# Optimization experiments

Measured on AMD Instinct MI355X. Metric: run time of the kernel, lower is better.

Reference implementation:

```python
import jax, jax.numpy as jnp
import numpy as np

EPS = 1e-8
TAU = 0.2  # gumbel temperature


def lorentz_linear(x, W, log_scale):
    # y = W x; project back onto hyperboloid (k=1): time from sigmoid, rescale space
    y = x @ W.T
    time = jax.nn.sigmoid(y[..., :1]) * jnp.exp(log_scale) + 1.1
    narrow = y[..., 1:]
    s = (time * time - 1.0) / jnp.clip(jnp.sum(narrow * narrow, axis=-1, keepdims=True), EPS, None)
    return jnp.concatenate([time, narrow * jnp.sqrt(s)], axis=-1)


def logmap0(x):
    # Lorentz (k=1) log map at origin o=(1,0,...,0): (0, arccosh(x0) * xs/||xs||)
    x0 = x[..., :1]
    xs = x[..., 1:]
    nrm = jnp.clip(jnp.linalg.norm(xs, axis=-1, keepdims=True), EPS, None)
    d = jnp.arccosh(jnp.clip(x0, 1.0 + 1e-6, None))
    return jnp.concatenate([jnp.zeros_like(x0), d * xs / nrm], axis=-1)


def lorentz_dist(a, b):
    # dist = arccosh(-<a,b>_L), <a,b>_L = -a0*b0 + sum_i ai*bi
    inner = a[..., 0] * b[..., 0] - jnp.sum(a[..., 1:] * b[..., 1:], axis=-1)
    return jnp.arccosh(jnp.clip(inner, 1.0 + 1e-6, None))


def scatter_softmax(score, seg, num_segments):
    m = jax.ops.segment_max(score, seg, num_segments=num_segments)
    m = jnp.where(jnp.isfinite(m), m, 0.0)  # empty segments
    e = jnp.exp(score - m[seg])
    s = jax.ops.segment_sum(e, seg, num_segments=num_segments)
    return e / jnp.clip(s[seg], EPS, None)


def setup_inputs() -> dict:
    key = jax.random.key(0)
    ks = jax.random.split(key, 8)
    N, E, D, A = 50000, 800000, 128, 128
    # nodes on hyperboloid: time = sqrt(1 + ||space||^2)
    xs = jax.random.normal(ks[0], (N, D - 1), dtype=jnp.float32)
    x0 = jnp.sqrt(1.0 + jnp.sum(xs * xs, axis=-1, keepdims=True))
    x = jnp.concatenate([x0, xs], axis=-1)
    src = jax.random.randint(ks[1], (E,), 0, N)
    dst = jax.random.randint(ks[2], (E,), 0, N)
    edge_value = jax.random.uniform(ks[3], (E,), dtype=jnp.float32)
    stdv = 1.0 / np.sqrt(D)
    Wq = jax.random.uniform(ks[4], (D, D), minval=-stdv, maxval=stdv, dtype=jnp.float32).at[:, 0].set(0.0)
    Wk = jax.random.uniform(ks[5], (D, D), minval=-stdv, maxval=stdv, dtype=jnp.float32).at[:, 0].set(0.0)
    Wa = jax.random.normal(ks[6], (A, D), dtype=jnp.float32) * np.sqrt(2.0 / (A + D))
    log_scale = jnp.asarray(np.log(10.0), dtype=jnp.float32)
    return {"x": x, "src": src, "dst": dst, "edge_value": edge_value,
            "Wq": Wq, "Wk": Wk, "Wa": Wa,
            "log_scale_q": log_scale, "log_scale_k": log_scale}


def reference(x, src, dst, edge_value, Wq, Wk, Wa, log_scale_q, log_scale_k):
    N = x.shape[0]
    # assignment logits in tangent space -> softmax
    ass = jax.nn.softmax(logmap0(x) @ Wa.T, axis=-1)  # [N, A]
    q = lorentz_linear(x, Wq, log_scale_q)            # [N, D]
    k = lorentz_linear(x, Wk, log_scale_k)
    # per-edge negative Lorentz distance
    score = -lorentz_dist(q[src], k[dst])             # [E]
    # scatter softmax over outgoing edges of each src node
    score = scatter_softmax(score, src, N)
    # sparse attention matmul: out[i] = sum_{e: src=i} score_e * ass[dst_e]
    ass = jax.ops.segment_sum(score[:, None] * ass[dst], src, num_segments=N)  # [N, A]
    # gumbel softmax on log(ass + 1e-6)
    logits = jnp.log(ass + 1e-6)
    u = jax.random.uniform(jax.random.key(42), logits.shape, minval=1e-10, maxval=1.0)
    g = -jnp.log(-jnp.log(u))
    return jax.nn.softmax((logits + g) / TAU, axis=-1)
```

## Files before the change

### kernel.cpp

```cpp
#include <hip/hip_runtime.h>
#include <hip/hip_bf16.h>
#include <hip/hip_fp16.h>
#include <math.h>


#define D128 128
#define XP 136

typedef _Float16 f16x2 __attribute__((ext_vector_type(2)));
typedef _Float16 f16x8 __attribute__((ext_vector_type(8)));
typedef float f32x4 __attribute__((ext_vector_type(4)));

union U4 { uint4 u; f16x2 f2[4]; __half2 hh[4]; };

__device__ __forceinline__ void threefry2x32(unsigned x0, unsigned x1,
                                             unsigned& o0, unsigned& o1) {
  const unsigned k0 = 0u, k1 = 42u;
  const unsigned k2 = 0x1BD11BDAu ^ k0 ^ k1;
  x0 += k0; x1 += k1;
#define TF_ROT(r) { x0 += x1; x1 = (x1 << (r)) | (x1 >> (32 - (r))); x1 ^= x0; }
  TF_ROT(13) TF_ROT(15) TF_ROT(26) TF_ROT(6)
  x0 += k1; x1 += k2 + 1u;
  TF_ROT(17) TF_ROT(29) TF_ROT(16) TF_ROT(24)
  x0 += k2; x1 += k0 + 2u;
  TF_ROT(13) TF_ROT(15) TF_ROT(26) TF_ROT(6)
  x0 += k0; x1 += k1 + 3u;
  TF_ROT(17) TF_ROT(29) TF_ROT(16) TF_ROT(24)
  x0 += k1; x1 += k2 + 4u;
  TF_ROT(13) TF_ROT(15) TF_ROT(26) TF_ROT(6)
  x0 += k2; x1 += k0 + 5u;
#undef TF_ROT
  o0 = x0; o1 = x1;
}

__global__ __launch_bounds__(256) void cvt_count_kernel(
    const float* __restrict__ Wq, const float* __restrict__ Wk,
    const float* __restrict__ Wa, __half* __restrict__ wqh,
    __half* __restrict__ wkh, __half* __restrict__ wah,
    const int* __restrict__ src, int* __restrict__ counts, int E) {
  int b = blockIdx.x;
  if (b < 24) {
    int i = b * 256 + threadIdx.x;
    int w = i >> 11, r = i & 2047;
    if (w >= 3) return;
    size_t off = (size_t)r * 8;
    const float* s = (w == 0) ? Wq : (w == 1) ? Wk : Wa;
    __half* d = (w == 0) ? wqh : (w == 1) ? wkh : wah;
    float4 a = *reinterpret_cast<const float4*>(s + off);
    float4 c = *reinterpret_cast<const float4*>(s + off + 4);
    union { __half2 h2[4]; uint4 u; } pk;
    pk.h2[0] = __floats2half2_rn(a.x, a.y);
    pk.h2[1] = __floats2half2_rn(a.z, a.w);
    pk.h2[2] = __floats2half2_rn(c.x, c.y);
    pk.h2[3] = __floats2half2_rn(c.z, c.w);
    *reinterpret_cast<uint4*>(d + off) = pk.u;
  } else {
    int e = (b - 24) * 256 + threadIdx.x;
    if (e < E) atomicAdd(&counts[src[e]], 1);
  }
}

__global__ __launch_bounds__(256) void gemm3_kernel(
    const float* __restrict__ X, const __half* __restrict__ wqh_g,
    const __half* __restrict__ wkh_g, const __half* __restrict__ wah_g,
    const float* __restrict__ lsq, const float* __restrict__ lsk,
    __half* __restrict__ qout, __half* __restrict__ kout,
    __half* __restrict__ aout, int N) {
  __shared__ __align__(16) _Float16 xs[64 * XP];
  __shared__ __align__(16) _Float16 wh[64 * XP];

  const int t = threadIdx.x;
  const int row0 = blockIdx.x * 64;

#pragma unroll
  for (int i = 0; i < 8; ++i) {
    int f = t + 256 * i, r = f >> 5, c4 = f & 31;
    float4 v = make_float4(0.f, 0.f, 0.f, 0.f);
    if (row0 + r < N)
      v = *reinterpret_cast<const float4*>(X + (size_t)(row0 + r) * D128 + c4 * 4);
    union { _Float16 h[4]; uint2 u; } p;
    p.h[0] = (_Float16)v.x; p.h[1] = (_Float16)v.y;
    p.h[2] = (_Float16)v.z; p.h[3] = (_Float16)v.w;
    *reinterpret_cast<uint2*>(&xs[r * XP + c4 * 4]) = p.u;
  }

  const int w = t >> 6, lane = t & 63;
  const int lc = lane & 15;
  const int arow = 16 * w + lc;
  const int koff = (lane >> 4) * 8;

  for (int m = 0; m < 3; ++m) {
    const __half* Wg = (m == 0) ? wqh_g : (m == 1) ? wkh_g : wah_g;

    if (m == 2) {
      __syncthreads();
#pragma unroll
      for (int rr = 0; rr < 2; ++rr) {
        int r = (t >> 3) + 32 * rr, tr = t & 7;
        U4 c0, c1;
        c0.u = *reinterpret_cast<uint4*>(&xs[r * XP + tr * 16]);
        c1.u = *reinterpret_cast<uint4*>(&xs[r * XP + tr * 16 + 8]);
        float v[16];
        float ss = 0.f;
#pragma unroll
        for (int j = 0; j < 4; ++j) {
          float2 f = __half22float2(c0.hh[j]);
          v[2 * j] = f.x; v[2 * j + 1] = f.y; ss += f.x * f.x + f.y * f.y;
        }
#pragma unroll
        for (int j = 0; j < 4; ++j) {
          float2 f = __half22float2(c1.hh[j]);
          v[8 + 2 * j] = f.x; v[9 + 2 * j] = f.y; ss += f.x * f.x + f.y * f.y;
        }
        if (tr == 0) ss -= v[0] * v[0];
#pragma unroll
        for (int msk = 1; msk < 8; msk <<= 1) ss += __shfl_xor(ss, msk);
        float x0v = __shfl(v[0], (t & 63) & ~7);
        float dd = acoshf(fmaxf(x0v, 1.f + 1e-6f));
        float sc = dd / fmaxf(sqrtf(ss), 1e-8f);
#pragma unroll
        for (int j = 0; j < 16; ++j) v[j] *= sc;
        if (tr == 0) v[0] = 0.f;
        union { __half2 h2[4]; uint4 u; } pk;
#pragma unroll
        for (int j = 0; j < 4; ++j) pk.h2[j] = __floats2half2_rn(v[2 * j], v[2 * j + 1]);
        *reinterpret_cast<uint4*>(&xs[r * XP + tr * 16]) = pk.u;
#pragma unroll
        for (int j = 0; j < 4; ++j) pk.h2[j] = __floats2half2_rn(v[8 + 2 * j], v[9 + 2 * j]);
        *reinterpret_cast<uint4*>(&xs[r * XP + tr * 16 + 8]) = pk.u;
      }
    }

    f32x4 acc[8];
#pragma unroll
    for (int i = 0; i < 8; ++i) acc[i] = (f32x4){0.f, 0.f, 0.f, 0.f};

    for (int h = 0; h < 2; ++h) {
      __syncthreads();
#pragma unroll
      for (int i = 0; i < 4; ++i) {
        int f = t + 256 * i, wr = f >> 4, c8 = f & 15;
        *reinterpret_cast<uint4*>(&wh[wr * XP + c8 * 8]) =
            *reinterpret_cast<const uint4*>(Wg + (size_t)(64 * h + wr) * D128 + c8 * 8);
      }
      __syncthreads();

#pragma unroll
      for (int kk = 0; kk < 4; ++kk) {
        f16x8 a = *reinterpret_cast<f16x8*>(&xs[arow * XP + kk * 32 + koff]);
#pragma unroll
        for (int tt = 0; tt < 4; ++tt) {
          f16x8 b = *reinterpret_cast<f16x8*>(&wh[(tt * 16 + lc) * XP + kk * 32 + koff]);
          acc[h * 4 + tt] =
              __builtin_amdgcn_mfma_f32_16x16x32_f16(a, b, acc[h * 4 + tt], 0, 0, 0);
        }
      }
    }

    if (m < 2) {
      float scale = expf(m ? lsk[0] : lsq[0]);
      __half* outp = m ? kout : qout;
      float sgn = m ? 1.f : -1.f;
#pragma unroll
      for (int j = 0; j < 4; ++j) {
        int gr = row0 + 16 * w + ((lane >> 4) << 2) + j;
        float ss = 0.f;
#pragma unroll
        for (int ct = 0; ct < 8; ++ct) {
          float v = acc[ct][j];
          if (ct == 0 && lc == 0) v = 0.f;
          ss += v * v;
        }
#pragma unroll
        for (int msk = 1; msk < 16; msk <<= 1) ss += __shfl_xor(ss, msk);
        float y0 = __shfl(acc[0][j], lane & ~15);
        float tm = scale / (1.f + expf(-y0)) + 1.1f;
        float qs = sqrtf((tm * tm - 1.f) / fmaxf(ss, 1e-8f)) * sgn;
        if (gr < N) {
#pragma unroll
          for (int ct = 0; ct < 8; ++ct) {
            float val = acc[ct][j] * qs;
            if (ct == 0 && lc == 0) val = tm;
            outp[(size_t)gr * D128 + ct * 16 + lc] = __float2half(val);
          }
        }
      }
    } else {
#pragma unroll
      for (int j = 0; j < 4; ++j) {
        int gr = row0 + 16 * w + ((lane >> 4) << 2) + j;
        float mx = acc[0][j];
#pragma unroll
        for (int ct = 1; ct < 8; ++ct) mx = fmaxf(mx, acc[ct][j]);
#pragma unroll
        for (int msk = 1; msk < 16; msk <<= 1) mx = fmaxf(mx, __shfl_xor(mx, msk));
        float e[8], sm = 0.f;
#pragma unroll
        for (int ct = 0; ct < 8; ++ct) { e[ct] = expf(acc[ct][j] - mx); sm += e[ct]; }
#pragma unroll
        for (int msk = 1; msk < 16; msk <<= 1) sm += __shfl_xor(sm, msk);
        float inv = 1.f / sm;
        if (gr < N) {
#pragma unroll
          for (int ct = 0; ct < 8; ++ct)
            aout[(size_t)gr * D128 + ct * 16 + lc] = __float2half(e[ct] * inv);
        }
      }
    }
  }
}

__global__ __launch_bounds__(256) void scan1_kernel(const int* __restrict__ counts,
                                                    int* __restrict__ incl,
                                                    int* __restrict__ partials, int N) {
  int i = blockIdx.x * 256 + threadIdx.x;
  int c = (i < N) ? counts[i] : 0;
  int lane = threadIdx.x & 63, w = threadIdx.x >> 6;
  int v = c;
#pragma unroll
  for (int d = 1; d < 64; d <<= 1) {
    int tv = __shfl_up(v, d);
    if (lane >= d) v += tv;
  }
  __shared__ int wsum[4];
  if (lane == 63) wsum[w] = v;
  __syncthreads();
  int add = 0;
  for (int j = 0; j < w; ++j) add += wsum[j];
  v += add;
  if (i < N) incl[i] = v;
  if (threadIdx.x == 255) partials[blockIdx.x] = v;
}

__global__ __launch_bounds__(256) void scan2_kernel(int* __restrict__ partials, int nparts) {
  int t = threadIdx.x;
  int p = (t < nparts) ? partials[t] : 0;
  int lane = t & 63, w = t >> 6;
  int v = p;
#pragma unroll
  for (int d = 1; d < 64; d <<= 1) {
    int tv = __shfl_up(v, d);
    if (lane >= d) v += tv;
  }
  __shared__ int wsum[4];
  if (lane == 63) wsum[w] = v;
  __syncthreads();
  int add = 0;
  for (int j = 0; j < w; ++j) add += wsum[j];
  v += add;
  if (t < nparts) partials[t] = v - p;
}

__global__ __launch_bounds__(256) void scan3_kernel(const int* __restrict__ counts,
                                                    int* __restrict__ incl_to_start,
                                                    int* __restrict__ cursor,
                                                    const int* __restrict__ partials, int N) {
  int i = blockIdx.x * 256 + threadIdx.x;
  if (i < N) {
    int s = incl_to_start[i] - counts[i] + partials[blockIdx.x];
    incl_to_start[i] = s;
    cursor[i] = s;
  }
}

__global__ __launch_bounds__(256) void csr_fill_kernel(
    const int* __restrict__ src, const int* __restrict__ dst,
    int* __restrict__ cursor, int* __restrict__ dst_s, int E) {
  int e = blockIdx.x * 256 + threadIdx.x;
  if (e < E) {
    int pos = atomicAdd(&cursor[src[e]], 1);
    dst_s[pos] = dst[e];
  }
}

__global__ __launch_bounds__(256) void node_fused_kernel(
    const __half* __restrict__ qh, const __half* __restrict__ kh,
    const __half* __restrict__ ass, const int* __restrict__ start,
    const int* __restrict__ counts, const int* __restrict__ dst_s,
    float* __restrict__ out, int N) {
  int n = blockIdx.x * 4 + (threadIdx.x >> 6);
  if (n >= N) return;
  int lane = threadIdx.x & 63;
  int g = lane >> 4, lq = lane & 15;
  int c8 = lq * 8;
  int st = start[n], deg = counts[n];

  U4 qv;
  qv.u = *reinterpret_cast<const uint4*>(qh + (size_t)n * D128 + c8);

  float lsum = 0.f;
  float acc[8];
#pragma unroll
  for (int j = 0; j < 8; ++j) acc[j] = 0.f;

  if (deg > 0) {
    int ecur = g;
    int dcur = dst_s[st + (ecur < deg ? ecur : 0)];
    U4 kv, av;
    kv.u = *reinterpret_cast<const uint4*>(kh + (size_t)dcur * D128 + c8);
    av.u = *reinterpret_cast<const uint4*>(ass + (size_t)dcur * D128 + c8);
    int nIter = (deg + 3) >> 2;

    for (int i = 0; i < nIter; ++i) {
      int enext = ecur + 4;
      int dnext = dst_s[st + (enext < deg ? enext : 0)];
      U4 kvn, avn;
      kvn.u = *reinterpret_cast<const uint4*>(kh + (size_t)dnext * D128 + c8);
      avn.u = *reinterpret_cast<const uint4*>(ass + (size_t)dnext * D128 + c8);

      float pa = __builtin_amdgcn_fdot2(qv.f2[0], kv.f2[0],
                 __builtin_amdgcn_fdot2(qv.f2[1], kv.f2[1], 0.f, false), false);
      float pb = __builtin_amdgcn_fdot2(qv.f2[2], kv.f2[2],
                 __builtin_amdgcn_fdot2(qv.f2[3], kv.f2[3], 0.f, false), false);
      float part = pa + pb;
#pragma unroll
      for (int msk = 1; msk < 16; msk <<= 1) part += __shfl_xor(part, msk);

      float x = fmaxf(part, 1.f + 1e-6f);
      float tt = x + sqrtf(__builtin_fmaf(x, x, -1.f));
      float w = __builtin_amdgcn_rcpf(tt);
      if (ecur >= deg) w = 0.f;

      lsum += w;
#pragma unroll
      for (int j = 0; j < 4; ++j) {
        acc[2 * j]     = fmaf(w, (float)av.f2[j][0], acc[2 * j]);
        acc[2 * j + 1] = fmaf(w, (float)av.f2[j][1], acc[2 * j + 1]);
      }

      kv = kvn; av = avn;
      ecur = enext;
    }
  }

#pragma unroll
  for (int j = 0; j < 8; ++j) {
    acc[j] += __shfl_xor(acc[j], 16);
    acc[j] += __shfl_xor(acc[j], 32);
  }
  lsum += __shfl_xor(lsum, 16);
  lsum += __shfl_xor(lsum, 32);

  float inv = (deg > 0) ? 1.f / fmaxf(lsum, 1e-8f) : 0.f;

  float vg[2];
#pragma unroll
  for (int jj = 0; jj < 2; ++jj) {
    int j = 2 * g + jj;
    unsigned o0, o1;
    threefry2x32(0u, (unsigned)(n * D128 + c8 + j), o0, o1);
    unsigned bits = o0 ^ o1;
    float f = __uint_as_float((bits >> 9) | 0x3f800000u) - 1.0f;
    float u = fmaxf(1e-10f, f * (1.0f - 1e-10f) + 1e-10f);
    float gmb = -logf(-logf(u));
    vg[jj] = (logf(acc[j] * inv + 1e-6f) + gmb) / 0.2f;
  }
  float mm = fmaxf(vg[0], vg[1]);
#pragma unroll
  for (int msk = 1; msk < 64; msk <<= 1) mm = fmaxf(mm, __shfl_xor(mm, msk));
  float e0 = expf(vg[0] - mm), e1 = expf(vg[1] - mm);
  float sm = e0 + e1;
#pragma unroll
  for (int msk = 1; msk < 64; msk <<= 1) sm += __shfl_xor(sm, msk);
  float invs = 1.f / sm;
  *reinterpret_cast<float2*>(out + (size_t)n * D128 + c8 + 2 * g) =
      make_float2(e0 * invs, e1 * invs);
}

extern "C" void kernel_launch(void* const* d_in, const int* in_sizes, int n_in,
                              void* d_out, int out_size, void* d_ws, size_t ws_size,
                              hipStream_t stream) {
  const float* x   = (const float*)d_in[0];
  const int*   src = (const int*)d_in[1];
  const int*   dst = (const int*)d_in[2];
  const float* Wq  = (const float*)d_in[4];
  const float* Wk  = (const float*)d_in[5];
  const float* Wa  = (const float*)d_in[6];
  const float* lsq = (const float*)d_in[7];
  const float* lsk = (const float*)d_in[8];
  const int N = in_sizes[0] / D128;
  const int E = in_sizes[1];
  float* out = (float*)d_out;

  __half* qh   = (__half*)d_ws;
  __half* kh   = qh + (size_t)N * D128;
  __half* ah   = kh + (size_t)N * D128;
  __half* wqh  = ah + (size_t)N * D128;
  __half* wkh  = wqh + 16384;
  __half* wah  = wkh + 16384;
  int* counts  = (int*)(wah + 16384);
  int* startv  = counts + N;
  int* cursor  = startv + N;
  int* partials= cursor + N;
  int* dst_s   = partials + 256;

  hipMemsetAsync(counts, 0, (size_t)N * sizeof(int), stream);

  const int eb = (E + 255) / 256;
  cvt_count_kernel<<<24 + eb, 256, 0, stream>>>(Wq, Wk, Wa, wqh, wkh, wah,
                                                src, counts, E);

  const int gemm_blocks = (N + 63) / 64;
  gemm3_kernel<<<gemm_blocks, 256, 0, stream>>>(x, wqh, wkh, wah, lsq, lsk,
                                                qh, kh, ah, N);

  const int nb = (N + 255) / 256;
  scan1_kernel<<<nb, 256, 0, stream>>>(counts, startv, partials, N);
  scan2_kernel<<<1, 256, 0, stream>>>(partials, nb);
  scan3_kernel<<<nb, 256, 0, stream>>>(counts, startv, cursor, partials, N);
  csr_fill_kernel<<<eb, 256, 0, stream>>>(src, dst, cursor, dst_s, E);

  node_fused_kernel<<<(N + 3) / 4, 256, 0, stream>>>(qh, kh, ah, startv,
                                                     counts, dst_s, out, N);
}
```

Baseline: 195.4 us.

## Split GEMM passes across grid dimension and precompute Gumbel noise separately

The three projection GEMMs (q, k, assignment) now run as separate blocks along blockIdx.y, each loading the full 128-row weight tile at once. This triples parallelism at the cost of reloading and converting X three times. Gumbel noise generation (threefry plus two logs) moves out of the node kernel into a standalone kernel that writes an N×128 float buffer, which the node kernel then reads back. This takes RNG compute off the tail of the node kernel but adds about 25 MB of extra memory traffic and a kernel launch.

```diff
diff --git a/kernel.cpp b/kernel.cpp
--- a/kernel.cpp
+++ b/kernel.cpp
@@ -60,6 +60,33 @@
   }
 }
 
+__global__ __launch_bounds__(256) void gumbel_pre_kernel(float* __restrict__ gmb,
+                                                         int total2) {
+  int i = blockIdx.x * 256 + threadIdx.x;
+  int stride = gridDim.x * 256;
+  for (; i < total2; i += stride) {
+    unsigned idx = (unsigned)(i * 2);
+    float2 r;
+    {
+      unsigned o0, o1;
+      threefry2x32(0u, idx, o0, o1);
+      unsigned bits = o0 ^ o1;
+      float f = __uint_as_float((bits >> 9) | 0x3f800000u) - 1.0f;
+      float u = fmaxf(1e-10f, f * (1.0f - 1e-10f) + 1e-10f);
+      r.x = -logf(-logf(u));
+    }
+    {
+      unsigned o0, o1;
+      threefry2x32(0u, idx + 1u, o0, o1);
+      unsigned bits = o0 ^ o1;
+      float f = __uint_as_float((bits >> 9) | 0x3f800000u) - 1.0f;
+      float u = fmaxf(1e-10f, f * (1.0f - 1e-10f) + 1e-10f);
+      r.y = -logf(-logf(u));
+    }
+    *reinterpret_cast<float2*>(gmb + idx) = r;
+  }
+}
+
 __global__ __launch_bounds__(256) void gemm3_kernel(
     const float* __restrict__ X, const __half* __restrict__ wqh_g,
     const __half* __restrict__ wkh_g, const __half* __restrict__ wah_g,
@@ -67,10 +94,11 @@
     __half* __restrict__ qout, __half* __restrict__ kout,
     __half* __restrict__ aout, int N) {
   __shared__ __align__(16) _Float16 xs[64 * XP];
-  __shared__ __align__(16) _Float16 wh[64 * XP];
+  __shared__ __align__(16) _Float16 wh[128 * XP];
 
   const int t = threadIdx.x;
   const int row0 = blockIdx.x * 64;
+  const int pass = blockIdx.y;
 
 #pragma unroll
   for (int i = 0; i < 8; ++i) {
@@ -88,123 +116,115 @@
   const int lc = lane & 15;
   const int arow = 16 * w + lc;
   const int koff = (lane >> 4) * 8;
-
-  for (int m = 0; m < 3; ++m) {
-    const __half* Wg = (m == 0) ? wqh_g : (m == 1) ? wkh_g : wah_g;
-
-    if (m == 2) {
-      __syncthreads();
-#pragma unroll
-      for (int rr = 0; rr < 2; ++rr) {
-        int r = (t >> 3) + 32 * rr, tr = t & 7;
-        U4 c0, c1;
-        c0.u = *reinterpret_cast<uint4*>(&xs[r * XP + tr * 16]);
-        c1.u = *reinterpret_cast<uint4*>(&xs[r * XP + tr * 16 + 8]);
-        float v[16];
-        float ss = 0.f;
-#pragma unroll
-        for (int j = 0; j < 4; ++j) {
-          float2 f = __half22float2(c0.hh[j]);
-          v[2 * j] = f.x; v[2 * j + 1] = f.y; ss += f.x * f.x + f.y * f.y;
+  const __half* Wg = (pass == 0) ? wqh_g : (pass == 1) ? wkh_g : wah_g;
+
+  if (pass == 2) {
+    __syncthreads();
+#pragma unroll
+    for (int rr = 0; rr < 2; ++rr) {
+      int r = (t >> 3) + 32 * rr, tr = t & 7;
+      U4 c0, c1;
+      c0.u = *reinterpret_cast<uint4*>(&xs[r * XP + tr * 16]);
+      c1.u = *reinterpret_cast<uint4*>(&xs[r * XP + tr * 16 + 8]);
+      float v[16];
+      float ss = 0.f;
+#pragma unroll
+      for (int j = 0; j < 4; ++j) {
+        float2 f = __half22float2(c0.hh[j]);
+        v[2 * j] = f.x; v[2 * j + 1] = f.y; ss += f.x * f.x + f.y * f.y;
+      }
+#pragma unroll
+      for (int j = 0; j < 4; ++j) {
+        float2 f = __half22float2(c1.hh[j]);
+        v[8 + 2 * j] = f.x; v[9 + 2 * j] = f.y; ss += f.x * f.x + f.y * f.y;
+      }
+      if (tr == 0) ss -= v[0] * v[0];
+#pragma unroll
+      for (int msk = 1; msk < 8; msk <<= 1) ss += __shfl_xor(ss, msk);
+      float x0v = __shfl(v[0], (t & 63) & ~7);
+      float dd = acoshf(fmaxf(x0v, 1.f + 1e-6f));
+      float sc = dd / fmaxf(sqrtf(ss), 1e-8f);
+#pragma unroll
+      for (int j = 0; j < 16; ++j) v[j] *= sc;
+      if (tr == 0) v[0] = 0.f;
+      union { __half2 h2[4]; uint4 u; } pk;
+#pragma unroll
+      for (int j = 0; j < 4; ++j) pk.h2[j] = __floats2half2_rn(v[2 * j], v[2 * j + 1]);
+      *reinterpret_cast<uint4*>(&xs[r * XP + tr * 16]) = pk.u;
+#pragma unroll
+      for (int j = 0; j < 4; ++j) pk.h2[j] = __floats2half2_rn(v[8 + 2 * j], v[9 + 2 * j]);
+      *reinterpret_cast<uint4*>(&xs[r * XP + tr * 16 + 8]) = pk.u;
+    }
+  }
+
+#pragma unroll
+  for (int i = 0; i < 8; ++i) {
+    int f = t + 256 * i, wr = f >> 4, c8 = f & 15;
+    *reinterpret_cast<uint4*>(&wh[wr * XP + c8 * 8]) =
+        *reinterpret_cast<const uint4*>(Wg + (size_t)wr * D128 + c8 * 8);
+  }
+  __syncthreads();
+
+  f32x4 acc[8];
+#pragma unroll
+  for (int i = 0; i < 8; ++i) acc[i] = (f32x4){0.f, 0.f, 0.f, 0.f};
+#pragma unroll
+  for (int kk = 0; kk < 4; ++kk) {
+    f16x8 a = *reinterpret_cast<f16x8*>(&xs[arow * XP + kk * 32 + koff]);
+#pragma unroll
+    for (int tt = 0; tt < 8; ++tt) {
+      f16x8 b = *reinterpret_cast<f16x8*>(&wh[(tt * 16 + lc) * XP + kk * 32 + koff]);
+      acc[tt] = __builtin_amdgcn_mfma_f32_16x16x32_f16(a, b, acc[tt], 0, 0, 0);
+    }
+  }
+
+  if (pass < 2) {
+    float scale = expf(pass ? lsk[0] : lsq[0]);
+    __half* outp = pass ? kout : qout;
+    float sgn = pass ? 1.f : -1.f;
+#pragma unroll
+    for (int j = 0; j < 4; ++j) {
+      int gr = row0 + 16 * w + ((lane >> 4) << 2) + j;
+      float ss = 0.f;
+#pragma unroll
+      for (int ct = 0; ct < 8; ++ct) {
+        float v = acc[ct][j];
+        if (ct == 0 && lc == 0) v = 0.f;
+        ss += v * v;
+      }
+#pragma unroll
+      for (int msk = 1; msk < 16; msk <<= 1) ss += __shfl_xor(ss, msk);
+      float y0 = __shfl(acc[0][j], lane & ~15);
+      float tm = scale / (1.f + expf(-y0)) + 1.1f;
+      float qs = sqrtf((tm * tm - 1.f) / fmaxf(ss, 1e-8f)) * sgn;
+      if (gr < N) {
+#pragma unroll
+        for (int ct = 0; ct < 8; ++ct) {
+          float val = acc[ct][j] * qs;
+          if (ct == 0 && lc == 0) val = tm;
+          outp[(size_t)gr * D128 + ct * 16 + lc] = __float2half(val);
         }
-#pragma unroll
-        for (int j = 0; j < 4; ++j) {
-          float2 f = __half22float2(c1.hh[j]);
-          v[8 + 2 * j] = f.x; v[9 + 2 * j] = f.y; ss += f.x * f.x + f.y * f.y;
-        }
-        if (tr == 0) ss -= v[0] * v[0];
-#pragma unroll
-        for (int msk = 1; msk < 8; msk <<= 1) ss += __shfl_xor(ss, msk);
-        float x0v = __shfl(v[0], (t & 63) & ~7);
-        float dd = acoshf(fmaxf(x0v, 1.f + 1e-6f));
-        float sc = dd / fmaxf(sqrtf(ss), 1e-8f);
-#pragma unroll
-        for (int j = 0; j < 16; ++j) v[j] *= sc;
-        if (tr == 0) v[0] = 0.f;
-        union { __half2 h2[4]; uint4 u; } pk;
-#pragma unroll
-        for (int j = 0; j < 4; ++j) pk.h2[j] = __floats2half2_rn(v[2 * j], v[2 * j + 1]);
-        *reinterpret_cast<uint4*>(&xs[r * XP + tr * 16]) = pk.u;
-#pragma unroll
-        for (int j = 0; j < 4; ++j) pk.h2[j] = __floats2half2_rn(v[8 + 2 * j], v[9 + 2 * j]);
-        *reinterpret_cast<uint4*>(&xs[r * XP + tr * 16 + 8]) = pk.u;
-      }
-    }
-
-    f32x4 acc[8];
-#pragma unroll
-    for (int i = 0; i < 8; ++i) acc[i] = (f32x4){0.f, 0.f, 0.f, 0.f};
-
-    for (int h = 0; h < 2; ++h) {
-      __syncthreads();
-#pragma unroll
-      for (int i = 0; i < 4; ++i) {
-        int f = t + 256 * i, wr = f >> 4, c8 = f & 15;
-        *reinterpret_cast<uint4*>(&wh[wr * XP + c8 * 8]) =
-            *reinterpret_cast<const uint4*>(Wg + (size_t)(64 * h + wr) * D128 + c8 * 8);
-      }
-      __syncthreads();
-
-#pragma unroll
-      for (int kk = 0; kk < 4; ++kk) {
-        f16x8 a = *reinterpret_cast<f16x8*>(&xs[arow * XP + kk * 32 + koff]);
-#pragma unroll
-        for (int tt = 0; tt < 4; ++tt) {
-          f16x8 b = *reinterpret_cast<f16x8*>(&wh[(tt * 16 + lc) * XP + kk * 32 + koff]);
-          acc[h * 4 + tt] =
-              __builtin_amdgcn_mfma_f32_16x16x32_f16(a, b, acc[h * 4 + tt], 0, 0, 0);
-        }
-      }
-    }
-
-    if (m < 2) {
-      float scale = expf(m ? lsk[0] : lsq[0]);
-      __half* outp = m ? kout : qout;
-      float sgn = m ? 1.f : -1.f;
-#pragma unroll
-      for (int j = 0; j < 4; ++j) {
-        int gr = row0 + 16 * w + ((lane >> 4) << 2) + j;
-        float ss = 0.f;
-#pragma unroll
-        for (int ct = 0; ct < 8; ++ct) {
-          float v = acc[ct][j];
-          if (ct == 0 && lc == 0) v = 0.f;
-          ss += v * v;
-        }
-#pragma unroll
-        for (int msk = 1; msk < 16; msk <<= 1) ss += __shfl_xor(ss, msk);
-        float y0 = __shfl(acc[0][j], lane & ~15);
-        float tm = scale / (1.f + expf(-y0)) + 1.1f;
-        float qs = sqrtf((tm * tm - 1.f) / fmaxf(ss, 1e-8f)) * sgn;
-        if (gr < N) {
-#pragma unroll
-          for (int ct = 0; ct < 8; ++ct) {
-            float val = acc[ct][j] * qs;
-            if (ct == 0 && lc == 0) val = tm;
-            outp[(size_t)gr * D128 + ct * 16 + lc] = __float2half(val);
-          }
-        }
-      }
-    } else {
-#pragma unroll
-      for (int j = 0; j < 4; ++j) {
-        int gr = row0 + 16 * w + ((lane >> 4) << 2) + j;
-        float mx = acc[0][j];
-#pragma unroll
-        for (int ct = 1; ct < 8; ++ct) mx = fmaxf(mx, acc[ct][j]);
-#pragma unroll
-        for (int msk = 1; msk < 16; msk <<= 1) mx = fmaxf(mx, __shfl_xor(mx, msk));
-        float e[8], sm = 0.f;
-#pragma unroll
-        for (int ct = 0; ct < 8; ++ct) { e[ct] = expf(acc[ct][j] - mx); sm += e[ct]; }
-#pragma unroll
-        for (int msk = 1; msk < 16; msk <<= 1) sm += __shfl_xor(sm, msk);
-        float inv = 1.f / sm;
-        if (gr < N) {
-#pragma unroll
-          for (int ct = 0; ct < 8; ++ct)
-            aout[(size_t)gr * D128 + ct * 16 + lc] = __float2half(e[ct] * inv);
-        }
+      }
+    }
+  } else {
+#pragma unroll
+    for (int j = 0; j < 4; ++j) {
+      int gr = row0 + 16 * w + ((lane >> 4) << 2) + j;
+      float mx = acc[0][j];
+#pragma unroll
+      for (int ct = 1; ct < 8; ++ct) mx = fmaxf(mx, acc[ct][j]);
+#pragma unroll
+      for (int msk = 1; msk < 16; msk <<= 1) mx = fmaxf(mx, __shfl_xor(mx, msk));
+      float e[8], sm = 0.f;
+#pragma unroll
+      for (int ct = 0; ct < 8; ++ct) { e[ct] = expf(acc[ct][j] - mx); sm += e[ct]; }
+#pragma unroll
+      for (int msk = 1; msk < 16; msk <<= 1) sm += __shfl_xor(sm, msk);
+      float inv = 1.f / sm;
+      if (gr < N) {
+#pragma unroll
+        for (int ct = 0; ct < 8; ++ct)
+          aout[(size_t)gr * D128 + ct * 16 + lc] = __float2half(e[ct] * inv);
       }
     }
   }
@@ -275,9 +295,9 @@
 
 __global__ __launch_bounds__(256) void node_fused_kernel(
     const __half* __restrict__ qh, const __half* __restrict__ kh,
-    const __half* __restrict__ ass, const int* __restrict__ start,
-    const int* __restrict__ counts, const int* __restrict__ dst_s,
-    float* __restrict__ out, int N) {
+    const __half* __restrict__ ass, const float* __restrict__ gmb,
+    const int* __restrict__ start, const int* __restrict__ counts,
+    const int* __restrict__ dst_s, float* __restrict__ out, int N) {
   int n = blockIdx.x * 4 + (threadIdx.x >> 6);
   if (n >= N) return;
   int lane = threadIdx.x & 63;
@@ -343,22 +363,14 @@
 
   float inv = (deg > 0) ? 1.f / fmaxf(lsum, 1e-8f) : 0.f;
 
-  float vg[2];
-#pragma unroll
-  for (int jj = 0; jj < 2; ++jj) {
-    int j = 2 * g + jj;
-    unsigned o0, o1;
-    threefry2x32(0u, (unsigned)(n * D128 + c8 + j), o0, o1);
-    unsigned bits = o0 ^ o1;
-    float f = __uint_as_float((bits >> 9) | 0x3f800000u) - 1.0f;
-    float u = fmaxf(1e-10f, f * (1.0f - 1e-10f) + 1e-10f);
-    float gmb = -logf(-logf(u));
-    vg[jj] = (logf(acc[j] * inv + 1e-6f) + gmb) / 0.2f;
-  }
-  float mm = fmaxf(vg[0], vg[1]);
+  float2 g2 = *reinterpret_cast<const float2*>(gmb + (size_t)n * D128 + c8 + 2 * g);
+  float vg0 = (logf(acc[2 * g] * inv + 1e-6f) + g2.x) / 0.2f;
+  float vg1 = (logf(acc[2 * g + 1] * inv + 1e-6f) + g2.y) / 0.2f;
+
+  float mm = fmaxf(vg0, vg1);
 #pragma unroll
   for (int msk = 1; msk < 64; msk <<= 1) mm = fmaxf(mm, __shfl_xor(mm, msk));
-  float e0 = expf(vg[0] - mm), e1 = expf(vg[1] - mm);
+  float e0 = expf(vg0 - mm), e1 = expf(vg1 - mm);
   float sm = e0 + e1;
 #pragma unroll
   for (int msk = 1; msk < 64; msk <<= 1) sm += __shfl_xor(sm, msk);
@@ -388,7 +400,8 @@
   __half* wqh  = ah + (size_t)N * D128;
   __half* wkh  = wqh + 16384;
   __half* wah  = wkh + 16384;
-  int* counts  = (int*)(wah + 16384);
+  float* gmb   = (float*)(wah + 16384);
+  int* counts  = (int*)(gmb + (size_t)N * D128);
   int* startv  = counts + N;
   int* cursor  = startv + N;
   int* partials= cursor + N;
@@ -399,10 +412,11 @@
   const int eb = (E + 255) / 256;
   cvt_count_kernel<<<24 + eb, 256, 0, stream>>>(Wq, Wk, Wa, wqh, wkh, wah,
                                                 src, counts, E);
+  gumbel_pre_kernel<<<2048, 256, 0, stream>>>(gmb, N * 64);
 
   const int gemm_blocks = (N + 63) / 64;
-  gemm3_kernel<<<gemm_blocks, 256, 0, stream>>>(x, wqh, wkh, wah, lsq, lsk,
-                                                qh, kh, ah, N);
+  gemm3_kernel<<<dim3(gemm_blocks, 3), 256, 0, stream>>>(x, wqh, wkh, wah,
+                                                         lsq, lsk, qh, kh, ah, N);
 
   const int nb = (N + 255) / 256;
   scan1_kernel<<<nb, 256, 0, stream>>>(counts, startv, partials, N);
@@ -410,6 +424,6 @@
   scan3_kernel<<<nb, 256, 0, stream>>>(counts, startv, cursor, partials, N);
   csr_fill_kernel<<<eb, 256, 0, stream>>>(src, dst, cursor, dst_s, E);
 
-  node_fused_kernel<<<(N + 3) / 4, 256, 0, stream>>>(qh, kh, ah, startv,
+  node_fused_kernel<<<(N + 3) / 4, 256, 0, stream>>>(qh, kh, ah, gmb, startv,
                                                      counts, dst_s, out, N);
 }
```

Measured after the change: 219.2 us. +12.2%, slower.
